# Optimization experiments

Hardware: AMD Instinct MI355X
Metric: run time of the kernel (lower is better)

The kernel has to match this reference:

```python
import jax, jax.numpy as jnp
import numpy as np

HIDDEN = 512
HEADS = 8
HEAD_DIM = HIDDEN // HEADS
INNER = int(HIDDEN * 4.0)
MAX_DIST = 512
LN_EPS = 1e-5


def _layernorm(x, g, b):
    mu = jnp.mean(x, axis=-1, keepdims=True)
    var = jnp.var(x, axis=-1, keepdims=True)
    return (x - mu) * jax.lax.rsqrt(var + LN_EPS) * g + b


def setup_inputs() -> dict:
    key = jax.random.key(0)
    ks = jax.random.split(key, 12)
    B, T = 4, 2048
    s = 0.02
    return {
        "x": jax.random.normal(ks[0], (B, T, HIDDEN), dtype=jnp.float32),
        "w_qkv": jax.random.normal(ks[1], (HIDDEN, 3 * HIDDEN), dtype=jnp.float32) * s,
        "b_qkv": jnp.zeros((3 * HIDDEN,), dtype=jnp.float32),
        "w_out": jax.random.normal(ks[2], (HIDDEN, HIDDEN), dtype=jnp.float32) * s,
        "b_out": jnp.zeros((HIDDEN,), dtype=jnp.float32),
        "ln1_g": jnp.ones((HIDDEN,), dtype=jnp.float32),
        "ln1_b": jnp.zeros((HIDDEN,), dtype=jnp.float32),
        "ln2_g": jnp.ones((HIDDEN,), dtype=jnp.float32),
        "ln2_b": jnp.zeros((HIDDEN,), dtype=jnp.float32),
        "w_mlp1": jax.random.normal(ks[3], (HIDDEN, INNER), dtype=jnp.float32) * s,
        "b_mlp1": jnp.zeros((INNER,), dtype=jnp.float32),
        "w_mlp2": jax.random.normal(ks[4], (INNER, HIDDEN), dtype=jnp.float32) * s,
        "b_mlp2": jnp.zeros((HIDDEN,), dtype=jnp.float32),
        "rel_table": jax.random.normal(ks[5], (2 * MAX_DIST + 1, HEADS), dtype=jnp.float32) * s,
    }


def reference(x, w_qkv, b_qkv, w_out, b_out, ln1_g, ln1_b, ln2_g, ln2_b,
              w_mlp1, b_mlp1, w_mlp2, b_mlp2, rel_table):
    B, T, C = x.shape
    scale = HEAD_DIM ** -0.5
    qkv = x @ w_qkv + b_qkv  # [B,T,3C]
    qkv = qkv.reshape(B, T, 3, HEADS, HEAD_DIM)
    q = qkv[:, :, 0].transpose(0, 2, 1, 3)  # [B,H,T,D]
    k = qkv[:, :, 1].transpose(0, 2, 1, 3)
    v = qkv[:, :, 2].transpose(0, 2, 1, 3)
    logits = jnp.einsum('bhqd,bhkd->bhqk', q, k) * scale
    # relative position bias: clamp(q_pos - k_pos) lookup -> [H,T,T]
    rel = jnp.clip(jnp.arange(T)[:, None] - jnp.arange(T)[None, :], -MAX_DIST, MAX_DIST) + MAX_DIST
    bias = rel_table[rel].transpose(2, 0, 1)  # [H,T,T]
    logits = logits + bias[None]
    attn = jax.nn.softmax(logits, axis=-1)
    out = jnp.einsum('bhqk,bhkd->bhqd', attn, v)
    out = out.transpose(0, 2, 1, 3).reshape(B, T, C)
    out = out @ w_out + b_out
    x = _layernorm(x + out, ln1_g, ln1_b)
    h = jax.nn.gelu(x @ w_mlp1 + b_mlp1, approximate=False)
    mlp_out = h @ w_mlp2 + b_mlp2
    return _layernorm(x + mlp_out, ln2_g, ln2_b)
```

## Files before the change

### kernel.cpp

```cpp
#include <hip/hip_runtime.h>
#include <hip/hip_bf16.h>

using bf16 = __hip_bfloat16;
typedef __attribute__((ext_vector_type(8))) short bf16x8;
typedef __attribute__((ext_vector_type(4))) short bf16x4;
typedef __attribute__((ext_vector_type(4))) float f32x4;

#define HIDDEN 512
#define HEADS 8
#define HDIM 64
#define INNER 2048
#define MAXD 512
#define BB 4
#define TT 2048
#define MM (BB*TT)
#define LOG2E 1.44269504088896340736f

typedef const __attribute__((address_space(1))) unsigned int* gas_u32p;
typedef __attribute__((address_space(3))) unsigned int* las_u32p;

__device__ __forceinline__ void gload_lds16(const void* g, void* l) {
    __builtin_amdgcn_global_load_lds((gas_u32p)g, (las_u32p)l, 16, 0, 0);
}
__device__ __forceinline__ short bfr(float x) {
    return (short)__bfloat16_as_ushort(__float2bfloat16(x));
}

__global__ __launch_bounds__(256) void cast_kernel(const float* __restrict__ in,
                                                   bf16* __restrict__ out) {
    int i = (blockIdx.x * 256 + threadIdx.x) * 4;
    float4 v = *(const float4*)&in[i];
    bf16 o[4] = {__float2bfloat16(v.x), __float2bfloat16(v.y),
                 __float2bfloat16(v.z), __float2bfloat16(v.w)};
    *(bf16x4*)&out[i] = *(bf16x4*)o;
}

__global__ __launch_bounds__(256) void wtrans_kernel(const float* __restrict__ in,
                                                     bf16* __restrict__ out,
                                                     int K, int N) {
    __shared__ float tile[32][33];
    int bx = blockIdx.x;
    int by = blockIdx.y;
    int lx = threadIdx.x & 31, ly = threadIdx.x >> 5;
    #pragma unroll
    for (int i = 0; i < 4; ++i)
        tile[ly + 8*i][lx] = in[(size_t)(by*32 + ly + 8*i) * N + bx*32 + lx];
    __syncthreads();
    #pragma unroll
    for (int i = 0; i < 4; ++i)
        out[(size_t)(bx*32 + ly + 8*i) * K + by*32 + lx] =
            __float2bfloat16(tile[lx][ly + 8*i]);
}

template<int EPI, int BN, int VT, int RESID>
__global__ __launch_bounds__(256) void gemm_kernel(
    const bf16* __restrict__ A, const bf16* __restrict__ BT,
    const float* __restrict__ bias, const float* __restrict__ resid,
    void* __restrict__ C, bf16* __restrict__ vt_out,
    int M, int N, int K)
{
    constexpr int NBF = BN / 32;
    constexpr int BBYTES = BN * 64;
    __shared__ __align__(16) bf16 As[2][128*32];
    __shared__ __align__(16) bf16 Bs[2][BN*32];
    const int tid = threadIdx.x;
    const int wid = tid >> 6;
    const int lane = tid & 63;
    const int lhi = lane >> 4, llo = lane & 15;
    const int m0 = blockIdx.x * 128, n0 = blockIdx.y * BN;
    const int wr = wid >> 1, wc = wid & 1;

    const int srow = tid >> 2, scol = (tid & 3) * 8;
    const bf16* Ap = A + (size_t)(m0 + srow) * K + scol;
    const bf16* Bp = BT + (size_t)(n0 + srow) * K + scol;
    const size_t step64 = (size_t)64 * K;

    f32x4 acc[4][NBF] = {};

    gload_lds16(Ap,          (char*)As + tid*16);
    gload_lds16(Ap + step64, (char*)As + 4096 + tid*16);
    gload_lds16(Bp,          (char*)Bs + tid*16);
    if (BN == 128) gload_lds16(Bp + step64, (char*)Bs + 4096 + tid*16);

    const int NK = K >> 5;
    for (int it = 0; it < NK; ++it) {
        const int p = it & 1;
        __syncthreads();
        if (it + 1 < NK) {
            const int k1 = (it + 1) << 5;
            gload_lds16(Ap + k1,          (char*)As + (p^1)*8192 + tid*16);
            gload_lds16(Ap + k1 + step64, (char*)As + (p^1)*8192 + 4096 + tid*16);
            gload_lds16(Bp + k1,          (char*)Bs + (p^1)*BBYTES + tid*16);
            if (BN == 128) gload_lds16(Bp + k1 + step64, (char*)Bs + (p^1)*BBYTES + 4096 + tid*16);
        }
        bf16x8 af[4], bfrg[NBF];
        #pragma unroll
        for (int ar = 0; ar < 4; ++ar)
            af[ar] = *(const bf16x8*)((const char*)As + p*8192 + (64*wr + 16*ar + llo)*64 + lhi*16);
        #pragma unroll
        for (int bc = 0; bc < NBF; ++bc)
            bfrg[bc] = *(const bf16x8*)((const char*)Bs + p*BBYTES + ((BN/2)*wc + 16*bc + llo)*64 + lhi*16);
        #pragma unroll
        for (int ar = 0; ar < 4; ++ar)
            #pragma unroll
            for (int bc = 0; bc < NBF; ++bc)
                acc[ar][bc] = __builtin_amdgcn_mfma_f32_16x16x32_bf16(
                    af[ar], bfrg[bc], acc[ar][bc], 0, 0, 0);
    }

    if (VT && n0 >= 1024) {
        #pragma unroll
        for (int ar = 0; ar < 4; ++ar) {
            const int row = m0 + 64*wr + 16*ar + 4*lhi;
            const int bq = row >> 11, t0 = row & 2047;
            #pragma unroll
            for (int bc = 0; bc < NBF; ++bc) {
                const int cv = n0 - 1024 + (BN/2)*wc + 16*bc + llo;
                const int h = cv >> 6, d = cv & 63;
                float bv = bias[n0 + (BN/2)*wc + 16*bc + llo];
                bf16x4 pk = {bfr(acc[ar][bc][0] + bv), bfr(acc[ar][bc][1] + bv),
                             bfr(acc[ar][bc][2] + bv), bfr(acc[ar][bc][3] + bv)};
                *(bf16x4*)&vt_out[(((size_t)(bq*8 + h) * 64 + d) << 11) + t0] = pk;
            }
        }
        return;
    }

    #pragma unroll
    for (int ar = 0; ar < 4; ++ar) {
        #pragma unroll
        for (int j = 0; j < 4; ++j) {
            int row = m0 + 64*wr + 16*ar + 4*lhi + j;
            #pragma unroll
            for (int bc = 0; bc < NBF; ++bc) {
                int col = n0 + (BN/2)*wc + 16*bc + llo;
                float v = acc[ar][bc][j] + bias[col];
                if (RESID) v += resid[(size_t)row * N + col];
                if (EPI == 2) {
                    float u = 0.7978845608028654f * (v + 0.044715f * v * v * v);
                    float e = __builtin_amdgcn_exp2f(u * (2.0f * LOG2E));
                    v = v * (1.0f - 1.0f / (1.0f + e));
                }
                if (EPI == 1)
                    ((float*)C)[(size_t)row * N + col] = v;
                else
                    ((bf16*)C)[(size_t)row * N + col] = __float2bfloat16(v);
            }
        }
    }
}

#define PTN (TT + 128)
__global__ __launch_bounds__(512) void attn_kernel(
    const bf16* __restrict__ qkv,
    const bf16* __restrict__ v_t,
    const float* __restrict__ rel_table,
    bf16* __restrict__ attn_out)
{
    __shared__ __align__(16) bf16 Ks[2][64*64];
    __shared__ __align__(16) bf16 Vs[2][64*64];
    __shared__ __align__(16) bf16 Ps[8][16*64];
    __shared__ float PT[PTN];

    const int qt = blockIdx.x, bh = blockIdx.y;
    const int b = bh >> 3, h = bh & 7;
    const int tid = threadIdx.x, wid = tid >> 6, lane = tid & 63;
    const int lhi = lane >> 4, llo = lane & 15;

    const int lo = qt * 128 - (TT - 1);
    for (int i = tid; i < PTN; i += 512) {
        int idx = min(max(i + lo, -MAXD), MAXD) + MAXD;
        PT[i] = rel_table[(size_t)idx * HEADS + h] * LOG2E;
    }

    const int q0w = qt * 128 + wid * 16;
    const int q = q0w + llo;
    bf16x8 bq[2];
    #pragma unroll
    for (int kc = 0; kc < 2; ++kc)
        bq[kc] = *(const bf16x8*)&qkv[(size_t)(b*TT + q) * 1536 + h*64 + kc*32 + lhi*8];

    const int so = tid * 16;
    const int r0 = so >> 7;
    const int c0 = (((so & 127) ^ ((r0 & 7) << 4)) >> 1);
    const bf16* kbase = qkv + (size_t)(b*TT) * 1536 + 512 + h*64;
    const bf16* vbase = v_t + (size_t)bh * 64 * TT;

    float accL = 0.f;
    f32x4 accO[4] = {};
    const int pti = wid*16 + llo + (TT - 1);

    gload_lds16(kbase + (size_t)r0 * 1536 + c0, (char*)Ks + so);
    gload_lds16(vbase + (size_t)r0 * TT + c0,   (char*)Vs + so);

    constexpr int NT = TT / 64;
    for (int kt = 0; kt < NT; ++kt) {
        const int p = kt & 1;
        const int kv0 = kt * 64;
        __syncthreads();
        if (kt + 1 < NT) {
            const int kn = kv0 + 64;
            gload_lds16(kbase + (size_t)(kn + r0) * 1536 + c0, (char*)Ks + (p^1)*8192 + so);
            gload_lds16(vbase + (size_t)r0 * TT + kn + c0,     (char*)Vs + (p^1)*8192 + so);
        }
        const char* Kb = (const char*)Ks + p*8192;
        const char* Vb = (const char*)Vs + p*8192;

        f32x4 s[4];
        __builtin_amdgcn_s_setprio(1);
        #pragma unroll
        for (int f = 0; f < 4; ++f) {
            f32x4 a = {};
            const int rr = 16*f + llo;
            #pragma unroll
            for (int kc = 0; kc < 2; ++kc) {
                bf16x8 ak = *(const bf16x8*)(Kb + rr*128 + (((4*kc + lhi) ^ (rr & 7)) << 4));
                a = __builtin_amdgcn_mfma_f32_16x16x32_bf16(ak, bq[kc], a, 0, 0, 0);
            }
            s[f] = a;
        }
        __builtin_amdgcn_s_setprio(0);

        const int ib = pti - kv0;
        #pragma unroll
        for (int f = 0; f < 4; ++f)
            #pragma unroll
            for (int j = 0; j < 4; ++j)
                s[f][j] = s[f][j] * (0.125f * LOG2E) + PT[ib - 16*f - 4*lhi - j];
        float tf[4];
        #pragma unroll
        for (int f = 0; f < 4; ++f) {
            float p0 = __builtin_amdgcn_exp2f(s[f][0]);
            float p1 = __builtin_amdgcn_exp2f(s[f][1]);
            float p2 = __builtin_amdgcn_exp2f(s[f][2]);
            float p3 = __builtin_amdgcn_exp2f(s[f][3]);
            tf[f] = (p0 + p1) + (p2 + p3);
            bf16x4 pk = {bfr(p0), bfr(p1), bfr(p2), bfr(p3)};
            *(bf16x4*)((char*)Ps + wid*2048 + llo*128 +
                       ((f*32 + lhi*8) ^ ((llo & 7) << 4))) = pk;
        }
        accL += (tf[0] + tf[1]) + (tf[2] + tf[3]);

        bf16x8 pf[2];
        #pragma unroll
        for (int kc = 0; kc < 2; ++kc)
            pf[kc] = *(const bf16x8*)((const char*)Ps + wid*2048 + llo*128 +
                                      ((kc*64 + lhi*16) ^ ((llo & 7) << 4)));
        __builtin_amdgcn_s_setprio(1);
        #pragma unroll
        for (int kc = 0; kc < 2; ++kc)
            #pragma unroll
            for (int f = 0; f < 4; ++f) {
                const int rr = 16*f + llo;
                bf16x8 av = *(const bf16x8*)(Vb + rr*128 + (((4*kc + lhi) ^ (rr & 7)) << 4));
                accO[f] = __builtin_amdgcn_mfma_f32_16x16x32_bf16(av, pf[kc], accO[f], 0, 0, 0);
            }
        __builtin_amdgcn_s_setprio(0);
    }

    accL += __shfl_xor(accL, 16, 64);
    accL += __shfl_xor(accL, 32, 64);
    const float rl = 1.0f / accL;
    const int row = b*TT + q;
    #pragma unroll
    for (int f = 0; f < 4; ++f) {
        bf16x4 ov = {bfr(accO[f][0] * rl), bfr(accO[f][1] * rl),
                     bfr(accO[f][2] * rl), bfr(accO[f][3] * rl)};
        *(bf16x4*)&attn_out[(size_t)row * HIDDEN + h*64 + 16*f + 4*lhi] = ov;
    }
}

template<int WB>
__global__ __launch_bounds__(256) void ln_kernel(
    const float* __restrict__ in,
    const float* __restrict__ g, const float* __restrict__ bb,
    float* __restrict__ of, bf16* __restrict__ ob)
{
    int row = blockIdx.x * 4 + (threadIdx.x >> 6);
    int lane = threadIdx.x & 63;
    const float* pa = in + (size_t)row * HIDDEN;
    float v[8];
    float s = 0.f, sq = 0.f;
    #pragma unroll
    for (int i = 0; i < 2; ++i) {
        float4 a4 = *(const float4*)&pa[lane*4 + i*256];
        v[i*4+0] = a4.x; v[i*4+1] = a4.y; v[i*4+2] = a4.z; v[i*4+3] = a4.w;
        #pragma unroll
        for (int j = 0; j < 4; ++j) { s += v[i*4+j]; sq += v[i*4+j]*v[i*4+j]; }
    }
    #pragma unroll
    for (int d = 1; d < 64; d <<= 1) {
        s  += __shfl_xor(s,  d, 64);
        sq += __shfl_xor(sq, d, 64);
    }
    float mean = s * (1.f / HIDDEN);
    float var  = sq * (1.f / HIDDEN) - mean * mean;
    float rstd = rsqrtf(var + 1e-5f);
    #pragma unroll
    for (int i = 0; i < 2; ++i)
        #pragma unroll
        for (int j = 0; j < 4; ++j) {
            int col = lane*4 + i*256 + j;
            float o = (v[i*4+j] - mean) * rstd * g[col] + bb[col];
            of[(size_t)row * HIDDEN + col] = o;
            if (WB) ob[(size_t)row * HIDDEN + col] = __float2bfloat16(o);
        }
}

extern "C" void kernel_launch(void* const* d_in, const int* in_sizes, int n_in,
                              void* d_out, int out_size, void* d_ws, size_t ws_size,
                              hipStream_t stream) {
    const float* x     = (const float*)d_in[0];
    const float* w_qkv = (const float*)d_in[1];
    const float* b_qkv = (const float*)d_in[2];
    const float* w_out = (const float*)d_in[3];
    const float* b_out = (const float*)d_in[4];
    const float* ln1_g = (const float*)d_in[5];
    const float* ln1_b = (const float*)d_in[6];
    const float* ln2_g = (const float*)d_in[7];
    const float* ln2_b = (const float*)d_in[8];
    const float* w1    = (const float*)d_in[9];
    const float* b1    = (const float*)d_in[10];
    const float* w2    = (const float*)d_in[11];
    const float* b2    = (const float*)d_in[12];
    const float* rel   = (const float*)d_in[13];
    float* out = (float*)d_out;

    char* ws = (char*)d_ws;
    bf16*  xb     = (bf16*)(ws + 0);
    bf16*  wqkv_t = (bf16*)(ws + 8388608);
    bf16*  wout_t = (bf16*)(ws + 9961472);
    bf16*  w1_t   = (bf16*)(ws + 10485760);
    bf16*  w2_t   = (bf16*)(ws + 12582912);
    bf16*  qkv    = (bf16*)(ws + 14680064);
    bf16*  v_t    = (bf16*)(ws + 39845888);
    bf16*  attn_o = (bf16*)(ws + 48234496);
    float* proj   = (float*)(ws + 56623104);
    float* x1     = (float*)(ws + 73400320);
    bf16*  x1b    = (bf16*)(ws + 90177536);
    bf16*  h      = (bf16*)(ws + 14680064);

    cast_kernel<<<MM*HIDDEN/4/256, 256, 0, stream>>>(x, xb);
    wtrans_kernel<<<dim3(1536/32, 512/32),  256, 0, stream>>>(w_qkv, wqkv_t, 512, 1536);
    wtrans_kernel<<<dim3(512/32,  512/32),  256, 0, stream>>>(w_out, wout_t, 512, 512);
    wtrans_kernel<<<dim3(2048/32, 512/32),  256, 0, stream>>>(w1,    w1_t,   512, 2048);
    wtrans_kernel<<<dim3(512/32,  2048/32), 256, 0, stream>>>(w2,    w2_t,   2048, 512);
    gemm_kernel<0,128,1,0><<<dim3(MM/128, 1536/128), 256, 0, stream>>>(
        xb, wqkv_t, b_qkv, nullptr, qkv, v_t, MM, 1536, 512);
    attn_kernel<<<dim3(TT/128, BB*HEADS), 512, 0, stream>>>(qkv, v_t, rel, attn_o);
    gemm_kernel<1,64,0,1><<<dim3(MM/128, 512/64), 256, 0, stream>>>(
        attn_o, wout_t, b_out, x, proj, nullptr, MM, 512, 512);
    ln_kernel<1><<<MM/4, 256, 0, stream>>>(proj, ln1_g, ln1_b, x1, x1b);
    gemm_kernel<2,128,0,0><<<dim3(MM/128, 2048/128), 256, 0, stream>>>(
        x1b, w1_t, b1, nullptr, h, nullptr, MM, 2048, 512);
    gemm_kernel<1,64,0,1><<<dim3(MM/128, 512/64), 256, 0, stream>>>(
        h, w2_t, b2, x1, proj, nullptr, MM, 512, 2048);
    ln_kernel<0><<<MM/4, 256, 0, stream>>>(proj, ln2_g, ln2_b, out, nullptr);
}
```

Baseline: 195.6 us.

## Swizzle GEMM LDS tiles and use constant bias outside clamp window in attention

```diff
diff --git a/kernel.cpp b/kernel.cpp
--- a/kernel.cpp
+++ b/kernel.cpp
@@ -70,10 +70,12 @@
     const int m0 = blockIdx.x * 128, n0 = blockIdx.y * BN;
     const int wr = wid >> 1, wc = wid & 1;
 
-    const int srow = tid >> 2, scol = (tid & 3) * 8;
+    const int srow = tid >> 2;
+    const int scol = ((tid & 3) ^ ((srow >> 1) & 3)) * 8;
     const bf16* Ap = A + (size_t)(m0 + srow) * K + scol;
     const bf16* Bp = BT + (size_t)(n0 + srow) * K + scol;
     const size_t step64 = (size_t)64 * K;
+    const int rsw = (llo >> 1) & 3;
 
     f32x4 acc[4][NBF] = {};
 
@@ -96,10 +98,12 @@
         bf16x8 af[4], bfrg[NBF];
         #pragma unroll
         for (int ar = 0; ar < 4; ++ar)
-            af[ar] = *(const bf16x8*)((const char*)As + p*8192 + (64*wr + 16*ar + llo)*64 + lhi*16);
+            af[ar] = *(const bf16x8*)((const char*)As + p*8192 +
+                       (64*wr + 16*ar + llo)*64 + ((lhi ^ rsw) << 4));
         #pragma unroll
         for (int bc = 0; bc < NBF; ++bc)
-            bfrg[bc] = *(const bf16x8*)((const char*)Bs + p*BBYTES + ((BN/2)*wc + 16*bc + llo)*64 + lhi*16);
+            bfrg[bc] = *(const bf16x8*)((const char*)Bs + p*BBYTES +
+                       ((BN/2)*wc + 16*bc + llo)*64 + ((lhi ^ rsw) << 4));
         #pragma unroll
         for (int ar = 0; ar < 4; ++ar)
             #pragma unroll
@@ -174,6 +178,7 @@
     }
 
     const int q0w = qt * 128 + wid * 16;
+    const int qb = qt * 128;
     const int q = q0w + llo;
     bf16x8 bq[2];
     #pragma unroll
@@ -192,12 +197,16 @@
 
     gload_lds16(kbase + (size_t)r0 * 1536 + c0, (char*)Ks + so);
     gload_lds16(vbase + (size_t)r0 * TT + c0,   (char*)Vs + so);
+    __syncthreads();
+
+    const float cFut  = PT[min(max(-512 - lo, 0), PTN - 1)];
+    const float cPast = PT[min(max( 512 - lo, 0), PTN - 1)];
 
     constexpr int NT = TT / 64;
     for (int kt = 0; kt < NT; ++kt) {
         const int p = kt & 1;
         const int kv0 = kt * 64;
-        __syncthreads();
+        if (kt) __syncthreads();
         if (kt + 1 < NT) {
             const int kn = kv0 + 64;
             gload_lds16(kbase + (size_t)(kn + r0) * 1536 + c0, (char*)Ks + (p^1)*8192 + so);
@@ -221,12 +230,28 @@
         }
         __builtin_amdgcn_s_setprio(0);
 
-        const int ib = pti - kv0;
-        #pragma unroll
-        for (int f = 0; f < 4; ++f)
-            #pragma unroll
-            for (int j = 0; j < 4; ++j)
-                s[f][j] = s[f][j] * (0.125f * LOG2E) + PT[ib - 16*f - 4*lhi - j];
+        const float sc = 0.125f * LOG2E;
+        if (kv0 >= qb + 640) {
+            #pragma unroll
+            for (int f = 0; f < 4; ++f)
+                #pragma unroll
+                for (int j = 0; j < 4; ++j)
+                    s[f][j] = fmaf(s[f][j], sc, cFut);
+        } else if (kv0 + 576 <= qb) {
+            #pragma unroll
+            for (int f = 0; f < 4; ++f)
+                #pragma unroll
+                for (int j = 0; j < 4; ++j)
+                    s[f][j] = fmaf(s[f][j], sc, cPast);
+        } else {
+            const int ib = pti - kv0;
+            #pragma unroll
+            for (int f = 0; f < 4; ++f)
+                #pragma unroll
+                for (int j = 0; j < 4; ++j)
+                    s[f][j] = fmaf(s[f][j], sc, PT[ib - 16*f - 4*lhi - j]);
+        }
+
         float tf[4];
         #pragma unroll
         for (int f = 0; f < 4; ++f) {
@@ -337,8 +362,8 @@
     bf16*  attn_o = (bf16*)(ws + 48234496);
     float* proj   = (float*)(ws + 56623104);
     float* x1     = (float*)(ws + 73400320);
+    bf16*  h      = (bf16*)(ws + 14680064);
     bf16*  x1b    = (bf16*)(ws + 90177536);
-    bf16*  h      = (bf16*)(ws + 14680064);
 
     cast_kernel<<<MM*HIDDEN/4/256, 256, 0, stream>>>(x, xb);
     wtrans_kernel<<<dim3(1536/32, 512/32),  256, 0, stream>>>(w_qkv, wqkv_t, 512, 1536);
```

Result: no change. 191.8 us (-2.0%).
